# Kernel optimization log

Measured on AMD Instinct MI355X. Metric: run time of the kernel, lower is better.

The kernel has to match this reference:

```python
import jax, jax.numpy as jnp
import numpy as np

N, D = 8192, 4096  # D must be a power of 2 for FWHT


def fwht(x):
    """Unnormalized Fast Walsh-Hadamard Transform along the last axis (len = 2^k)."""
    orig_shape = x.shape
    d = orig_shape[-1]
    x = x.reshape(-1, d)
    h = 1
    while h < d:
        x = x.reshape(-1, d // (2 * h), 2, h)
        a = x[..., 0, :]
        b = x[..., 1, :]
        x = jnp.stack([a + b, a - b], axis=-2)
        h *= 2
    return x.reshape(orig_shape)


def setup_inputs() -> dict:
    key = jax.random.key(0)
    k = jax.random.split(key, 6)
    return {
        "x": jax.random.normal(k[0], (N, D), dtype=jnp.float32),
        "s1": jax.random.normal(k[1], (D,), dtype=jnp.float32),
        "s2": jax.random.normal(k[2], (D,), dtype=jnp.float32),
        "g_mu": jax.random.normal(k[3], (D,), dtype=jnp.float32),
        "g_rho": jax.random.normal(k[4], (D,), dtype=jnpp.float32) if False else jax.random.normal(k[4], (D,), dtype=jnp.float32),
        "epsilon": jax.random.normal(k[5], (D,), dtype=jnp.float32),
    }


def reference(x, s1, s2, g_mu, g_rho, epsilon):
    # W(u) = diag(s1) H diag(u) H diag(s2); forward (sample=True):
    #   b = x @ W(g_mu).T + x @ W(softplus(g_rho) * epsilon).T
    # Per-row (H symmetric): x @ W(u).T = s1 * fwht(u * fwht(s2 * x)).
    t = fwht(x * s2)                                  # [N, D], shared between both terms
    g_noise = jax.nn.softplus(g_rho) * epsilon        # g_sigma_sqrt @ epsilon
    b = s1 * fwht(t * g_mu) + s1 * fwht(t * g_noise)  # [N, D]
    return b
```

## Files before the change

### kernel.cpp

```cpp
#include <hip/hip_runtime.h>
#include <math.h>

#define D 4096
#define WPB 4

__device__ __forceinline__ void fwht64(float* v) {
#pragma unroll
    for (int h = 1; h < 64; h <<= 1) {
#pragma unroll
        for (int i = 0; i < 64; i += 2 * h) {
#pragma unroll
            for (int j = i; j < i + h; ++j) {
                const float a = v[j];
                const float b = v[j + h];
                v[j]     = a + b;
                v[j + h] = a - b;
            }
        }
    }
}

__global__ void whvi_prep(const float* __restrict__ g_mu,
                          const float* __restrict__ g_rho,
                          const float* __restrict__ eps,
                          float* __restrict__ gq) {
    const int i = blockIdx.x * 64 + threadIdx.x;
    const int l = i >> 6, k = i & 63;
    const int e = (l & 3) | (k << 2) | ((l >> 2) << 8);
    const float r  = g_rho[e];
    const float sp = (r > 20.f) ? r : log1pf(expf(r));
    gq[i] = g_mu[e] + sp * eps[e];
}

__global__ void __launch_bounds__(WPB * 64) whvi_main(
    const float* __restrict__ x,  const float* __restrict__ s1,
    const float* __restrict__ s2, const float* __restrict__ gq,
    const float* __restrict__ g_mu, const float* __restrict__ g_rho,
    const float* __restrict__ eps, float* __restrict__ out, int rows) {
    __shared__ alignas(16) float lds_all[WPB * D];
    const int tid = threadIdx.x;
    const int w = tid >> 6;
    const int l = tid & 63;
    float* lds = lds_all + (w << 12);
    const long long row = (long long)blockIdx.x * WPB + w;
    if (row >= rows) return;
    const float* xr = x + row * (long long)D;
    float v[64];

#pragma unroll
    for (int q = 0; q < 16; ++q) {
        const int base = (l << 2) + (q << 8);
        const float4 xv = *reinterpret_cast<const float4*>(xr + base);
        const float4 sv = *reinterpret_cast<const float4*>(s2 + base);
        v[4 * q + 0] = xv.x * sv.x;
        v[4 * q + 1] = xv.y * sv.y;
        v[4 * q + 2] = xv.z * sv.z;
        v[4 * q + 3] = xv.w * sv.w;
    }

    fwht64(v);

#pragma unroll
    for (int q = 0; q < 16; ++q) {
        const int addr = ((l ^ (q & 7)) << 2) + (q << 8);
        *reinterpret_cast<float4*>(&lds[addr]) =
            make_float4(v[4 * q], v[4 * q + 1], v[4 * q + 2], v[4 * q + 3]);
    }
    __syncthreads();
    {
        const int xb = (l & 3) | ((l >> 2) << 8);
        const int mk = (l >> 2) & 7;
#pragma unroll
        for (int k = 0; k < 64; ++k)
            v[k] = lds[xb + ((k ^ mk) << 2)];
    }

    fwht64(v);

    if (gq) {
#pragma unroll
        for (int m = 0; m < 16; ++m) {
            const float4 gv = *reinterpret_cast<const float4*>(gq + l * 64 + 4 * m);
            v[4 * m + 0] *= gv.x;
            v[4 * m + 1] *= gv.y;
            v[4 * m + 2] *= gv.z;
            v[4 * m + 3] *= gv.w;
        }
    } else {
#pragma unroll
        for (int k = 0; k < 64; ++k) {
            const int e = (l & 3) | (k << 2) | ((l >> 2) << 8);
            const float r  = g_rho[e];
            const float sp = (r > 20.f) ? r : log1pf(expf(r));
            v[k] *= g_mu[e] + sp * eps[e];
        }
    }

    fwht64(v);

    __syncthreads();
    {
        const int xb = (l & 3) | ((l >> 2) << 8);
        const int mk = (l >> 2) & 7;
#pragma unroll
        for (int k = 0; k < 64; ++k)
            lds[xb + ((k ^ mk) << 2)] = v[k];
    }
    __syncthreads();
#pragma unroll
    for (int q = 0; q < 16; ++q) {
        const int addr = ((l ^ (q & 7)) << 2) + (q << 8);
        const float4 t = *reinterpret_cast<const float4*>(&lds[addr]);
        v[4 * q + 0] = t.x;
        v[4 * q + 1] = t.y;
        v[4 * q + 2] = t.z;
        v[4 * q + 3] = t.w;
    }

    fwht64(v);

    float* outr = out + row * (long long)D;
#pragma unroll
    for (int q = 0; q < 16; ++q) {
        const int base = (l << 2) + (q << 8);
        const float4 sv = *reinterpret_cast<const float4*>(s1 + base);
        float4 o;
        o.x = v[4 * q + 0] * sv.x;
        o.y = v[4 * q + 1] * sv.y;
        o.z = v[4 * q + 2] * sv.z;
        o.w = v[4 * q + 3] * sv.w;
        *reinterpret_cast<float4*>(outr + base) = o;
    }
}

extern "C" void kernel_launch(void* const* d_in, const int* in_sizes, int n_in,
                              void* d_out, int out_size, void* d_ws, size_t ws_size,
                              hipStream_t stream) {
    const float* x     = (const float*)d_in[0];
    const float* s1    = (const float*)d_in[1];
    const float* s2    = (const float*)d_in[2];
    const float* g_mu  = (const float*)d_in[3];
    const float* g_rho = (const float*)d_in[4];
    const float* eps   = (const float*)d_in[5];
    float* out = (float*)d_out;
    const int rows = in_sizes[0] / D;

    float* gq = nullptr;
    if (ws_size >= (size_t)D * sizeof(float)) {
        gq = (float*)d_ws;
        whvi_prep<<<D / 64, 64, 0, stream>>>(g_mu, g_rho, eps, gq);
    }
    const int blocks = (rows + WPB - 1) / WPB;
    whvi_main<<<blocks, 64 * WPB, 0, stream>>>(x, s1, s2, gq, g_mu, g_rho, eps, out, rows);
}
```

Before: 267.7 us.

## Use persistent grid-stride waves with next-row prefetch and wave-local LDS sync

The main kernel now launches a fixed grid of 256 blocks of 8 waves. Each wave loops over rows in grid-stride fashion and prefetches the next row of x into registers while transforming the current row. Block-wide __syncthreads are replaced by s_waitcnt lgkmcnt(0), since each wave only touches its own LDS slice. This aims to hide global load latency and remove barrier stalls, at the cost of 64 extra registers per lane for the prefetch buffer and 128KB of LDS per block, which may limit occupancy.

```diff
diff --git a/kernel.cpp b/kernel.cpp
--- a/kernel.cpp
+++ b/kernel.cpp
@@ -2,7 +2,8 @@
 #include <math.h>
 
 #define D 4096
-#define WPB 4
+#define WPB 8
+#define NBLK 256
 
 __device__ __forceinline__ void fwht64(float* v) {
 #pragma unroll
@@ -32,104 +33,118 @@
     gq[i] = g_mu[e] + sp * eps[e];
 }
 
-__global__ void __launch_bounds__(WPB * 64) whvi_main(
+__global__ void __launch_bounds__(WPB * 64, 2) whvi_main(
     const float* __restrict__ x,  const float* __restrict__ s1,
     const float* __restrict__ s2, const float* __restrict__ gq,
     const float* __restrict__ g_mu, const float* __restrict__ g_rho,
     const float* __restrict__ eps, float* __restrict__ out, int rows) {
     __shared__ alignas(16) float lds_all[WPB * D];
     const int tid = threadIdx.x;
-    const int w = tid >> 6;
-    const int l = tid & 63;
+    const int w   = tid >> 6;
+    const int l   = tid & 63;
     float* lds = lds_all + (w << 12);
-    const long long row = (long long)blockIdx.x * WPB + w;
+    const int gw = blockIdx.x * WPB + w;
+    const int nw = gridDim.x * WPB;
+    const int xb = (l & 3) | ((l >> 2) << 8);
+    const int mk = (l >> 2) & 7;
+
+    long long row = gw;
     if (row >= rows) return;
-    const float* xr = x + row * (long long)D;
-    float v[64];
+
+    float4 xn[16];
+    {
+        const float* xr = x + row * (long long)D;
+#pragma unroll
+        for (int q = 0; q < 16; ++q)
+            xn[q] = *reinterpret_cast<const float4*>(xr + (l << 2) + (q << 8));
+    }
+
+    while (row < rows) {
+        const long long next = row + nw;
+        float v[64];
 
 #pragma unroll
-    for (int q = 0; q < 16; ++q) {
-        const int base = (l << 2) + (q << 8);
-        const float4 xv = *reinterpret_cast<const float4*>(xr + base);
-        const float4 sv = *reinterpret_cast<const float4*>(s2 + base);
-        v[4 * q + 0] = xv.x * sv.x;
-        v[4 * q + 1] = xv.y * sv.y;
-        v[4 * q + 2] = xv.z * sv.z;
-        v[4 * q + 3] = xv.w * sv.w;
-    }
+        for (int q = 0; q < 16; ++q) {
+            const float4 sv = *reinterpret_cast<const float4*>(s2 + (l << 2) + (q << 8));
+            v[4 * q + 0] = xn[q].x * sv.x;
+            v[4 * q + 1] = xn[q].y * sv.y;
+            v[4 * q + 2] = xn[q].z * sv.z;
+            v[4 * q + 3] = xn[q].w * sv.w;
+        }
+        if (next < rows) {
+            const float* xr2 = x + next * (long long)D;
+#pragma unroll
+            for (int q = 0; q < 16; ++q)
+                xn[q] = *reinterpret_cast<const float4*>(xr2 + (l << 2) + (q << 8));
+        }
 
-    fwht64(v);
+        fwht64(v);
 
 #pragma unroll
-    for (int q = 0; q < 16; ++q) {
-        const int addr = ((l ^ (q & 7)) << 2) + (q << 8);
-        *reinterpret_cast<float4*>(&lds[addr]) =
-            make_float4(v[4 * q], v[4 * q + 1], v[4 * q + 2], v[4 * q + 3]);
-    }
-    __syncthreads();
-    {
-        const int xb = (l & 3) | ((l >> 2) << 8);
-        const int mk = (l >> 2) & 7;
+        for (int q = 0; q < 16; ++q) {
+            const int addr = ((l ^ (q & 7)) << 2) + (q << 8);
+            *reinterpret_cast<float4*>(&lds[addr]) =
+                make_float4(v[4 * q], v[4 * q + 1], v[4 * q + 2], v[4 * q + 3]);
+        }
+        asm volatile("s_waitcnt lgkmcnt(0)" ::: "memory");
 #pragma unroll
         for (int k = 0; k < 64; ++k)
             v[k] = lds[xb + ((k ^ mk) << 2)];
-    }
 
-    fwht64(v);
+        fwht64(v);
 
-    if (gq) {
+        if (gq) {
 #pragma unroll
-        for (int m = 0; m < 16; ++m) {
-            const float4 gv = *reinterpret_cast<const float4*>(gq + l * 64 + 4 * m);
-            v[4 * m + 0] *= gv.x;
-            v[4 * m + 1] *= gv.y;
-            v[4 * m + 2] *= gv.z;
-            v[4 * m + 3] *= gv.w;
+            for (int m = 0; m < 16; ++m) {
+                const float4 gv = *reinterpret_cast<const float4*>(gq + l * 64 + 4 * m);
+                v[4 * m + 0] *= gv.x;
+                v[4 * m + 1] *= gv.y;
+                v[4 * m + 2] *= gv.z;
+                v[4 * m + 3] *= gv.w;
+            }
+        } else {
+#pragma unroll
+            for (int k = 0; k < 64; ++k) {
+                const int e = (l & 3) | (k << 2) | ((l >> 2) << 8);
+                const float r  = g_rho[e];
+                const float sp = (r > 20.f) ? r : log1pf(expf(r));
+                v[k] *= g_mu[e] + sp * eps[e];
+            }
         }
-    } else {
-#pragma unroll
-        for (int k = 0; k < 64; ++k) {
-            const int e = (l & 3) | (k << 2) | ((l >> 2) << 8);
-            const float r  = g_rho[e];
-            const float sp = (r > 20.f) ? r : log1pf(expf(r));
-            v[k] *= g_mu[e] + sp * eps[e];
-        }
-    }
 
-    fwht64(v);
+        fwht64(v);
 
-    __syncthreads();
-    {
-        const int xb = (l & 3) | ((l >> 2) << 8);
-        const int mk = (l >> 2) & 7;
+        asm volatile("s_waitcnt lgkmcnt(0)" ::: "memory");
 #pragma unroll
         for (int k = 0; k < 64; ++k)
             lds[xb + ((k ^ mk) << 2)] = v[k];
-    }
-    __syncthreads();
+        asm volatile("s_waitcnt lgkmcnt(0)" ::: "memory");
 #pragma unroll
-    for (int q = 0; q < 16; ++q) {
-        const int addr = ((l ^ (q & 7)) << 2) + (q << 8);
-        const float4 t = *reinterpret_cast<const float4*>(&lds[addr]);
-        v[4 * q + 0] = t.x;
-        v[4 * q + 1] = t.y;
-        v[4 * q + 2] = t.z;
-        v[4 * q + 3] = t.w;
-    }
+        for (int q = 0; q < 16; ++q) {
+            const int addr = ((l ^ (q & 7)) << 2) + (q << 8);
+            const float4 t = *reinterpret_cast<const float4*>(&lds[addr]);
+            v[4 * q + 0] = t.x;
+            v[4 * q + 1] = t.y;
+            v[4 * q + 2] = t.z;
+            v[4 * q + 3] = t.w;
+        }
+        asm volatile("s_waitcnt lgkmcnt(0)" ::: "memory");
 
-    fwht64(v);
+        fwht64(v);
 
-    float* outr = out + row * (long long)D;
+        float* outr = out + row * (long long)D;
 #pragma unroll
-    for (int q = 0; q < 16; ++q) {
-        const int base = (l << 2) + (q << 8);
-        const float4 sv = *reinterpret_cast<const float4*>(s1 + base);
-        float4 o;
-        o.x = v[4 * q + 0] * sv.x;
-        o.y = v[4 * q + 1] * sv.y;
-        o.z = v[4 * q + 2] * sv.z;
-        o.w = v[4 * q + 3] * sv.w;
-        *reinterpret_cast<float4*>(outr + base) = o;
+        for (int q = 0; q < 16; ++q) {
+            const float4 sv = *reinterpret_cast<const float4*>(s1 + (l << 2) + (q << 8));
+            float4 o;
+            o.x = v[4 * q + 0] * sv.x;
+            o.y = v[4 * q + 1] * sv.y;
+            o.z = v[4 * q + 2] * sv.z;
+            o.w = v[4 * q + 3] * sv.w;
+            *reinterpret_cast<float4*>(outr + (l << 2) + (q << 8)) = o;
+        }
+
+        row = next;
     }
 }
 
@@ -150,6 +165,5 @@
         gq = (float*)d_ws;
         whvi_prep<<<D / 64, 64, 0, stream>>>(g_mu, g_rho, eps, gq);
     }
-    const int blocks = (rows + WPB - 1) / WPB;
-    whvi_main<<<blocks, 64 * WPB, 0, stream>>>(x, s1, s2, gq, g_mu, g_rho, eps, out, rows);
+    whvi_main<<<NBLK, WPB * 64, 0, stream>>>(x, s1, s2, gq, g_mu, g_rho, eps, out, rows);
 }
```

After: 387.8 us. 44.8% more time.
